# Optimization experiments

Hardware: AMD Instinct MI355X
Metric: run time of the kernel (lower is better)

## Reference

```python
import math
import jax, jax.numpy as jnp
import numpy as np

NQ = 10      # n_qubits
NB = 4       # n_blocks (angle encoding layers)
VD = 6       # vqc_depth (hardware-efficient layers)
LAT = 128    # latent_dim
NOBS = 9     # n_qubits - k_local + 1 sliding 2-local groups
DIM = 2 ** NQ


def sin_embed(t, dim):
    half = dim // 2
    freqs = jnp.exp(-math.log(10000.0) * jnp.arange(half, dtype=jnp.float32) / half)
    args = t[:, None] * freqs[None, :]
    return jnp.concatenate([jnp.cos(args), jnp.sin(args)], axis=-1)


def apply_ry(psi, theta, q):
    # psi: [B, 2^NQ] complex; theta: scalar or [B]
    B = psi.shape[0]
    p = psi.reshape(B, 2 ** q, 2, 2 ** (NQ - 1 - q))
    th = jnp.broadcast_to(theta, (B,))
    c = jnp.cos(th / 2)[:, None, None].astype(psi.dtype)
    s = jnp.sin(th / 2)[:, None, None].astype(psi.dtype)
    p0, p1 = p[:, :, 0, :], p[:, :, 1, :]
    return jnp.stack([c * p0 - s * p1, s * p0 + c * p1], axis=2).reshape(B, -1)


def apply_cnot(psi, ctrl, tgt):
    B = psi.shape[0]
    pt = psi.reshape((B,) + (2,) * NQ)
    p0 = jax.lax.index_in_dim(pt, 0, axis=ctrl + 1, keepdims=True)
    p1 = jnp.flip(jax.lax.index_in_dim(pt, 1, axis=ctrl + 1, keepdims=True), axis=tgt + 1)
    return jnp.concatenate([p0, p1], axis=ctrl + 1).reshape(B, -1)


def run_circuit(enc, var_params):
    B = enc.shape[0]
    psi = jnp.zeros((B, DIM), dtype=jnp.complex64).at[:, 0].set(1.0)
    # angle encoding: RY data re-uploading blocks with CNOT ladders between blocks
    for layer in range(NB):
        for q in range(NQ):
            psi = apply_ry(psi, enc[:, layer * NQ + q], q)
        if layer < NB - 1:
            for q in range(0, NQ - 1, 2):
                psi = apply_cnot(psi, q, q + 1)
            for q in range(1, NQ - 1, 2):
                psi = apply_cnot(psi, q, q + 1)
    # hardware-efficient variational layers
    for ly in range(VD):
        for q in range(NQ):
            psi = apply_ry(psi, var_params[ly, q], q)
        for q in range(0, NQ - 1, 2):
            psi = apply_cnot(psi, q, q + 1)
        for q in range(1, NQ - 1, 2):
            psi = apply_cnot(psi, q, q + 1)
    return psi


def build_H(A_p, B_p, D_p):
    # create_Hermitian: lower-tri (row-major) = A + iB; h[i-1,i-1] = D[i]; H = h + h^dagger
    r, c = np.tril_indices(4, -1)  # order matches count+j loop: (1,0),(2,0),(2,1),(3,0),(3,1),(3,2)
    L = jnp.zeros((NOBS, 4, 4), dtype=jnp.complex64)
    L = L.at[:, r, c].set(A_p.astype(jnp.complex64) + 1j * B_p.astype(jnp.complex64))
    d = 2.0 * jnp.concatenate([D_p[:, 1:4], jnp.zeros((NOBS, 1), dtype=D_p.dtype)], axis=1)
    H = L + jnp.conj(jnp.swapaxes(L, 1, 2))
    H = H + jax.vmap(jnp.diag)(d).astype(jnp.complex64)
    return H


def expvals(psi, H):
    B = psi.shape[0]
    outs = []
    for s in range(NOBS):  # sliding window [s, s+1]
        pg = psi.reshape(B, 2 ** s, 4, 2 ** (NQ - s - 2))
        outs.append(jnp.einsum('balr,lk,bakr->b', jnp.conj(pg), H[s], pg).real)
    return jnp.stack(outs, axis=-1)


def setup_inputs() -> dict:
    ks = jax.random.split(jax.random.key(0), 12)
    B = 2048
    return {
        'z_t': jax.random.normal(ks[0], (B, LAT), dtype=jnp.float32),
        't': jax.random.uniform(ks[1], (B,), dtype=jnp.float32),
        'W1': 0.05 * jax.random.normal(ks[2], (2 * LAT, 256), dtype=jnp.float32),
        'b1': jnp.zeros((256,), dtype=jnp.float32),
        'W2': 0.05 * jax.random.normal(ks[3], (256, NB * NQ), dtype=jnp.float32),
        'b2': jnp.zeros((NB * NQ,), dtype=jnp.float32),
        'var_params': 0.01 * jax.random.normal(ks[4], (VD, NQ), dtype=jnp.float32),
        'A_p': 2.0 * jax.random.normal(ks[5], (NOBS, 6), dtype=jnp.float32),
        'B_p': 2.0 * jax.random.normal(ks[6], (NOBS, 6), dtype=jnp.float32),
        'D_p': 2.0 * jax.random.normal(ks[7], (NOBS, 4), dtype=jnp.float32),
        'W3': 0.05 * jax.random.normal(ks[8], (NOBS, 256), dtype=jnp.float32),
        'b3': jnp.zeros((256,), dtype=jnp.float32),
        'W4': 0.05 * jax.random.normal(ks[9], (256, LAT), dtype=jnp.float32),
        'b4': jnp.zeros((LAT,), dtype=jnp.float32),
    }


def reference(z_t, t, W1, b1, W2, b2, var_params, A_p, B_p, D_p, W3, b3, W4, b4):
    x = jnp.concatenate([z_t, sin_embed(t, LAT)], axis=-1)   # [B, 2*LAT]
    h = jax.nn.silu(x @ W1 + b1)
    enc = h @ W2 + b2                                         # [B, NB*NQ]
    psi = run_circuit(enc, var_params)                        # [B, 2^NQ]
    obs = expvals(psi, build_H(A_p, B_p, D_p))                # [B, NOBS]
    return jax.nn.silu(obs @ W3 + b3) @ W4 + b4               # [B, LAT]
```

## Files before the change

### kernel.cpp

```cpp
#include <hip/hip_runtime.h>
#include <math.h>

#define NOBS 9
#define LATD 128

typedef float f2 __attribute__((ext_vector_type(2)));

__device__ __forceinline__ float silu_f(float x) { return x / (1.f + expf(-x)); }
__device__ __forceinline__ f2 splat2(float x) { return (f2){x, x}; }
__device__ __forceinline__ f2 fma2(f2 a, f2 b, f2 c) { return __builtin_elementwise_fma(a, b, c); }


template<int CTRL>
__device__ __forceinline__ float dpp_perm(float x) {
  return __int_as_float(__builtin_amdgcn_update_dpp(0, __float_as_int(x), CTRL, 0xF, 0xF, true));
}
template<int PAT>
__device__ __forceinline__ float ds_swz(float x) {
  return __int_as_float(__builtin_amdgcn_ds_swizzle(__float_as_int(x), PAT));
}
__device__ __forceinline__ float x4f(float x) { return ds_swz<0x101F>(x); }

__device__ __forceinline__ float wave_sum(float x) {
  x += dpp_perm<0xB1>(x);
  x += dpp_perm<0x4E>(x);
  x += x4f(x);
  x += dpp_perm<0x128>(x);
  x += ds_swz<0x401F>(x);
  x += __shfl_xor(x, 32, 64);
  return x;
}


template<int M>
__device__ __forceinline__ void ry_reg(float v[16], float c, float s) {
#pragma unroll
  for (int r = 0; r < 16; ++r) {
    if ((r & M) == 0) {
      float p0 = v[r], p1 = v[r | M];
      v[r]     = c * p0 - s * p1;
      v[r | M] = s * p0 + c * p1;
    }
  }
}

__device__ __forceinline__ void apply_rys(float v[16], int lane,
                                          const float* __restrict__ cc,
                                          const float* __restrict__ ss) {
  ry_reg<8>(v, cc[0], ss[0]);
  ry_reg<4>(v, cc[1], ss[1]);
  ry_reg<2>(v, cc[2], ss[2]);
  ry_reg<1>(v, cc[3], ss[3]);
  { float c = cc[4], s = ss[4], sp = (lane & 32) ? s : -s;
#pragma unroll
    for (int r = 0; r < 16; ++r) { float p = __shfl_xor(v[r], 32, 64); v[r] = fmaf(c, v[r], sp * p); } }
  { float c = cc[5], s = ss[5], sp = (lane & 16) ? s : -s;
#pragma unroll
    for (int r = 0; r < 16; ++r) { float p = __shfl_xor(v[r], 16, 64); v[r] = fmaf(c, v[r], sp * p); } }
  { float c = cc[6], s = ss[6], sp = (lane & 8) ? s : -s;
#pragma unroll
    for (int r = 0; r < 16; ++r) { float p = dpp_perm<0x128>(v[r]); v[r] = fmaf(c, v[r], sp * p); } }
  { float c = cc[7], s = ss[7], sp = (lane & 4) ? s : -s;
#pragma unroll
    for (int r = 0; r < 16; ++r) { float p = x4f(v[r]); v[r] = fmaf(c, v[r], sp * p); } }
  { float c = cc[8], s = ss[8], sp = (lane & 2) ? s : -s;
#pragma unroll
    for (int r = 0; r < 16; ++r) { float p = dpp_perm<0x4E>(v[r]); v[r] = fmaf(c, v[r], sp * p); } }
  { float c = cc[9], s = ss[9], sp = (lane & 1) ? s : -s;
#pragma unroll
    for (int r = 0; r < 16; ++r) { float p = dpp_perm<0xB1>(v[r]); v[r] = fmaf(c, v[r], sp * p); } }
}

__device__ __forceinline__ void cnot_ladder(float v[16], int lane) {
  float t;
  t=v[8];  v[8]=v[12];  v[12]=t;
  t=v[9];  v[9]=v[13];  v[13]=t;
  t=v[10]; v[10]=v[14]; v[14]=t;
  t=v[11]; v[11]=v[15]; v[15]=t;
  t=v[2];  v[2]=v[3];   v[3]=t;
  t=v[6];  v[6]=v[7];   v[7]=t;
  t=v[10]; v[10]=v[11]; v[11]=t;
  t=v[14]; v[14]=v[15]; v[15]=t;
  int se = lane ^ ((lane & 42) >> 1);
#pragma unroll
  for (int r = 0; r < 16; ++r) v[r] = __shfl(v[r], se, 64);
  t=v[4];  v[4]=v[6];   v[6]=t;
  t=v[5];  v[5]=v[7];   v[7]=t;
  t=v[12]; v[12]=v[14]; v[14]=t;
  t=v[13]; v[13]=v[15]; v[15]=t;
  int so  = lane ^ ((lane & 20) >> 1);
  int so1 = so ^ 32;
#pragma unroll
  for (int r = 0; r < 16; ++r) v[r] = __shfl(v[r], (r & 1) ? so1 : so, 64);
}


__global__ __launch_bounds__(256) void fused_kernel(
    const float* __restrict__ z, const float* __restrict__ t,
    const float* __restrict__ W1, const float* __restrict__ b1,
    const float* __restrict__ W2, const float* __restrict__ b2,
    const float* __restrict__ varp,
    const float* __restrict__ A_p, const float* __restrict__ D_p,
    const float* __restrict__ W3, const float* __restrict__ b3,
    const float* __restrict__ W4, const float* __restrict__ b4,
    float* __restrict__ out) {
  __shared__ f2    xsA[256], xsB[256];
  __shared__ float hs[4][256];
  __shared__ f2    hp[2][256];
  __shared__ float dump[4][1024];
  __shared__ float cs[4][40], sn[4][40];
  __shared__ float vcs[60], vsn[60];
  __shared__ float os[4][NOBS];

  int tid = threadIdx.x;
  int b0 = blockIdx.x * 4;

  if (tid < 60) {
    float s, c;
    sincosf(0.5f * varp[tid], &s, &c);
    vcs[tid] = c; vsn[tid] = s;
  }

  if (tid < 128) {
#pragma unroll
    for (int r = 0; r < 4; ++r) {
      float val = z[(b0 + r) * 128 + tid];
      if (r < 2) ((float*)xsA)[2 * tid + r]       = val;
      else       ((float*)xsB)[2 * tid + (r - 2)] = val;
    }
  } else {
    int i = tid - 128, j = i & 63;
    float freq = expf(-9.2103403719761836f * (float)j * (1.f / 64.f));
#pragma unroll
    for (int r = 0; r < 4; ++r) {
      float arg = t[b0 + r] * freq;
      float val = (i < 64) ? cosf(arg) : sinf(arg);
      int k = 128 + i;
      if (r < 2) ((float*)xsA)[2 * k + r]       = val;
      else       ((float*)xsB)[2 * k + (r - 2)] = val;
    }
  }
  __syncthreads();

  {
    f2 a01 = splat2(b1[tid]), a23 = a01;
    float w[16];
#pragma unroll
    for (int j = 0; j < 16; ++j) w[j] = W1[j * 256 + tid];
#pragma unroll 1
    for (int k0 = 0; k0 < 256; k0 += 16) {
      int kn = (k0 + 16) & 255;
      float wn[16];
#pragma unroll
      for (int j = 0; j < 16; ++j) wn[j] = W1[(kn + j) * 256 + tid];
#pragma unroll
      for (int j = 0; j < 16; ++j) {
        a01 = fma2(xsA[k0 + j], splat2(w[j]), a01);
        a23 = fma2(xsB[k0 + j], splat2(w[j]), a23);
      }
#pragma unroll
      for (int j = 0; j < 16; ++j) w[j] = wn[j];
    }
    hs[0][tid] = silu_f(a01.x);
    hs[1][tid] = silu_f(a01.y);
    hs[2][tid] = silu_f(a23.x);
    hs[3][tid] = silu_f(a23.y);
  }
  __syncthreads();

  if (tid < 160) {
    int r = tid / 40, c = tid - r * 40;
    float acc = b2[c];
    float w[16];
#pragma unroll
    for (int j = 0; j < 16; ++j) w[j] = W2[j * 40 + c];
#pragma unroll 1
    for (int k0 = 0; k0 < 256; k0 += 16) {
      int kn = (k0 + 16) & 255;
      float wn[16];
#pragma unroll
      for (int j = 0; j < 16; ++j) wn[j] = W2[(kn + j) * 40 + c];
#pragma unroll
      for (int j = 0; j < 16; ++j) acc = fmaf(hs[r][k0 + j], w[j], acc);
#pragma unroll
      for (int j = 0; j < 16; ++j) w[j] = wn[j];
    }
    float s, cv;
    sincosf(0.5f * acc, &s, &cv);
    cs[r][c] = cv; sn[r][c] = s;
  }
  __syncthreads();

  {
    int wave = tid >> 6;
    int lane = tid & 63;
    const float* cc = cs[wave];
    const float* ss = sn[wave];

    float base = 1.f;
    base *= (lane & 32) ? ss[4] : cc[4];
    base *= (lane & 16) ? ss[5] : cc[5];
    base *= (lane & 8)  ? ss[6] : cc[6];
    base *= (lane & 4)  ? ss[7] : cc[7];
    base *= (lane & 2)  ? ss[8] : cc[8];
    base *= (lane & 1)  ? ss[9] : cc[9];
    float v[16];
#pragma unroll
    for (int r = 0; r < 16; ++r) {
      float p = base;
      p *= (r & 8) ? ss[0] : cc[0];
      p *= (r & 4) ? ss[1] : cc[1];
      p *= (r & 2) ? ss[2] : cc[2];
      p *= (r & 1) ? ss[3] : cc[3];
      v[r] = p;
    }
    cnot_ladder(v, lane);
#pragma unroll 1
    for (int layer = 1; layer < 4; ++layer) {
      apply_rys(v, lane, cc + layer * 10, ss + layer * 10);
      if (layer < 3) cnot_ladder(v, lane);
    }
#pragma unroll 1
    for (int ly = 0; ly < 6; ++ly) {
      apply_rys(v, lane, vcs + ly * 10, vsn + ly * 10);
      cnot_ladder(v, lane);
    }

    float* sw = dump[wave];
#pragma unroll
    for (int r = 0; r < 16; ++r) sw[r * 64 + lane] = v[r];

#pragma unroll 1
    for (int s = 0; s < NOBS; ++s) {
      const int r8 = 8 - s;
      const int stride = 1 << r8;
      float h10 = A_p[s*6+0], h20 = A_p[s*6+1], h21 = A_p[s*6+2];
      float h30 = A_p[s*6+3], h31 = A_p[s*6+4], h32 = A_p[s*6+5];
      float d0 = 2.f * D_p[s*4+1], d1 = 2.f * D_p[s*4+2], d2 = 2.f * D_p[s*4+3];
      float acc = 0.f;
#pragma unroll
      for (int k = 0; k < 4; ++k) {
        int p = lane + 64 * k;
        int a  = p >> r8;
        int rr = p & (stride - 1);
        int bse = (a << (r8 + 2)) + rr;
        float x0 = sw[bse];
        float x1 = sw[bse + stride];
        float x2 = sw[bse + 2 * stride];
        float x3 = sw[bse + 3 * stride];
        acc += d0 * x0 * x0 + d1 * x1 * x1 + d2 * x2 * x2
             + 2.f * (h10 * x1 * x0 + h20 * x2 * x0 + h21 * x2 * x1
                    + h30 * x3 * x0 + h31 * x3 * x1 + h32 * x3 * x2);
      }
      acc = wave_sum(acc);
      if (lane == 0) os[wave][s] = acc;
    }
  }
  __syncthreads();

  {
    f2 a01 = splat2(b3[tid]), a23 = a01;
#pragma unroll
    for (int s = 0; s < NOBS; ++s) {
      float wv = W3[s * 256 + tid];
      a01 = fma2((f2){os[0][s], os[1][s]}, splat2(wv), a01);
      a23 = fma2((f2){os[2][s], os[3][s]}, splat2(wv), a23);
    }
    hp[0][tid] = (f2){silu_f(a01.x), silu_f(a01.y)};
    hp[1][tid] = (f2){silu_f(a23.x), silu_f(a23.y)};
  }
  __syncthreads();

  {
    int c = tid & 127, rg = tid >> 7;
    const f2* hr = hp[rg];
    f2 acc = splat2(b4[c]);
    float w[16];
#pragma unroll
    for (int j = 0; j < 16; ++j) w[j] = W4[j * 128 + c];
#pragma unroll 1
    for (int k0 = 0; k0 < 256; k0 += 16) {
      int kn = (k0 + 16) & 255;
      float wn[16];
#pragma unroll
      for (int j = 0; j < 16; ++j) wn[j] = W4[(kn + j) * 128 + c];
#pragma unroll
      for (int j = 0; j < 16; ++j) acc = fma2(hr[k0 + j], splat2(w[j]), acc);
#pragma unroll
      for (int j = 0; j < 16; ++j) w[j] = wn[j];
    }
    out[(b0 + rg * 2) * LATD + c]     = acc.x;
    out[(b0 + rg * 2 + 1) * LATD + c] = acc.y;
  }
}


extern "C" void kernel_launch(void* const* d_in, const int* in_sizes, int n_in,
                              void* d_out, int out_size, void* d_ws, size_t ws_size,
                              hipStream_t stream) {
  const float* z_t  = (const float*)d_in[0];
  const float* t    = (const float*)d_in[1];
  const float* W1   = (const float*)d_in[2];
  const float* b1   = (const float*)d_in[3];
  const float* W2   = (const float*)d_in[4];
  const float* b2   = (const float*)d_in[5];
  const float* varp = (const float*)d_in[6];
  const float* A_p  = (const float*)d_in[7];
  const float* D_p  = (const float*)d_in[9];
  const float* W3   = (const float*)d_in[10];
  const float* b3   = (const float*)d_in[11];
  const float* W4   = (const float*)d_in[12];
  const float* b4   = (const float*)d_in[13];
  float* out = (float*)d_out;

  int B = in_sizes[1];

  fused_kernel<<<B / 4, 256, 0, stream>>>(z_t, t, W1, b1, W2, b2, varp,
                                          A_p, D_p, W3, b3, W4, b4, out);
}
```

Measured before the change: 124.2 us.

## Stream weights into LDS via async global_load_lds ring buffers and split W4 over K

Weights W1, W2, W3 and W4 are now copied with global_load_lds into one flat LDS arena. W1 and W4 stream through a three-slot per-wave ring gated by vmcnt waits, instead of register double-buffering from global memory. The W4 GEMV is split across waves by K halves, with partial sums reduced through LDS, so all four waves work on it. LDS regions are aliased (the state dump reuses the W2 region) and launch bounds ask for two blocks per CU. The aim is to hide global load latency and cut register pressure, at the cost of fragile manual waitcnt scheduling and a larger LDS footprint.

After: 132.0 us. 1.06x slower.

```diff
diff --git a/kernel.cpp b/kernel.cpp
--- a/kernel.cpp
+++ b/kernel.cpp
@@ -1,8 +1,8 @@
 #include <hip/hip_runtime.h>
 #include <math.h>
+#include <stdint.h>
 
 #define NOBS 9
-#define LATD 128
 
 typedef float f2 __attribute__((ext_vector_type(2)));
 
@@ -10,6 +10,16 @@
 __device__ __forceinline__ f2 splat2(float x) { return (f2){x, x}; }
 __device__ __forceinline__ f2 fma2(f2 a, f2 b, f2 c) { return __builtin_elementwise_fma(a, b, c); }
 
+typedef const __attribute__((address_space(1))) uint32_t* gas_t;
+typedef __attribute__((address_space(3))) uint32_t* las_t;
+__device__ __forceinline__ void gl4(const float* g, float* l) {
+  __builtin_amdgcn_global_load_lds((gas_t)g, (las_t)l, 4, 0, 0);
+}
+__device__ __forceinline__ void gl16(const float* g, float* l) {
+  __builtin_amdgcn_global_load_lds((gas_t)g, (las_t)l, 16, 0, 0);
+}
+#define WAITVM(N) do { asm volatile("s_waitcnt vmcnt(" #N ")" ::: "memory"); \
+                       __builtin_amdgcn_sched_barrier(0); } while (0)
 
 template<int CTRL>
 __device__ __forceinline__ float dpp_perm(float x) {
@@ -30,7 +40,6 @@
   x += __shfl_xor(x, 32, 64);
   return x;
 }
-
 
 template<int M>
 __device__ __forceinline__ void ry_reg(float v[16], float c, float s) {
@@ -94,8 +103,22 @@
   for (int r = 0; r < 16; ++r) v[r] = __shfl(v[r], (r & 1) ? so1 : so, 64);
 }
 
-
-__global__ __launch_bounds__(256) void fused_kernel(
+#define RING 0
+#define XS   6144
+#define HS   7168
+#define W2O  8192
+#define W3O  12288
+#define HP4O 14592
+#define PARTO 15616
+#define CS   18432
+#define SN   18592
+#define VCS  18752
+#define VSN  18816
+#define OSB  18880
+#define LDSF 18944
+
+
+__global__ __launch_bounds__(256, 2) void fused_kernel(
     const float* __restrict__ z, const float* __restrict__ t,
     const float* __restrict__ W1, const float* __restrict__ b1,
     const float* __restrict__ W2, const float* __restrict__ b2,
@@ -104,98 +127,111 @@
     const float* __restrict__ W3, const float* __restrict__ b3,
     const float* __restrict__ W4, const float* __restrict__ b4,
     float* __restrict__ out) {
-  __shared__ f2    xsA[256], xsB[256];
-  __shared__ float hs[4][256];
-  __shared__ f2    hp[2][256];
-  __shared__ float dump[4][1024];
-  __shared__ float cs[4][40], sn[4][40];
-  __shared__ float vcs[60], vsn[60];
-  __shared__ float os[4][NOBS];
-
-  int tid = threadIdx.x;
-  int b0 = blockIdx.x * 4;
-
+  __shared__ __align__(16) float lds[LDSF];
+  float4* xs4 = (float4*)(lds + XS);
+  float4* hp4 = (float4*)(lds + HP4O);
+  float4* part4 = (float4*)(lds + PARTO);
+
+  const int tid  = threadIdx.x;
+  const int b0   = blockIdx.x * 4;
+  const int w    = tid >> 6;
+  const int lane = tid & 63;
+  const int c0   = w * 64;
+  const int ringw = w * 1536;
+
+  if (tid < 128) {
+    int k = tid;
+    xs4[k] = (float4){z[(b0 + 0) * 128 + k], z[(b0 + 1) * 128 + k],
+                      z[(b0 + 2) * 128 + k], z[(b0 + 3) * 128 + k]};
+  } else {
+    int i = tid - 128, j = i & 63;
+    float freq = expf(-9.2103403719761836f * (float)j * (1.f / 64.f));
+    float a0 = t[b0] * freq, a1 = t[b0 + 1] * freq, a2 = t[b0 + 2] * freq, a3 = t[b0 + 3] * freq;
+    float4 xv = (i < 64) ? (float4){cosf(a0), cosf(a1), cosf(a2), cosf(a3)}
+                         : (float4){sinf(a0), sinf(a1), sinf(a2), sinf(a3)};
+    xs4[128 + i] = xv;
+  }
   if (tid < 60) {
     float s, c;
     sincosf(0.5f * varp[tid], &s, &c);
-    vcs[tid] = c; vsn[tid] = s;
-  }
-
-  if (tid < 128) {
-#pragma unroll
-    for (int r = 0; r < 4; ++r) {
-      float val = z[(b0 + r) * 128 + tid];
-      if (r < 2) ((float*)xsA)[2 * tid + r]       = val;
-      else       ((float*)xsB)[2 * tid + (r - 2)] = val;
-    }
-  } else {
-    int i = tid - 128, j = i & 63;
-    float freq = expf(-9.2103403719761836f * (float)j * (1.f / 64.f));
-#pragma unroll
-    for (int r = 0; r < 4; ++r) {
-      float arg = t[b0 + r] * freq;
-      float val = (i < 64) ? cosf(arg) : sinf(arg);
-      int k = 128 + i;
-      if (r < 2) ((float*)xsA)[2 * k + r]       = val;
-      else       ((float*)xsB)[2 * k + (r - 2)] = val;
-    }
+    lds[VCS + tid] = c; lds[VSN + tid] = s;
   }
   __syncthreads();
 
   {
-    f2 a01 = splat2(b1[tid]), a23 = a01;
-    float w[16];
-#pragma unroll
-    for (int j = 0; j < 16; ++j) w[j] = W1[j * 256 + tid];
-#pragma unroll 1
-    for (int k0 = 0; k0 < 256; k0 += 16) {
-      int kn = (k0 + 16) & 255;
-      float wn[16];
-#pragma unroll
-      for (int j = 0; j < 16; ++j) wn[j] = W1[(kn + j) * 256 + tid];
-#pragma unroll
-      for (int j = 0; j < 16; ++j) {
-        a01 = fma2(xsA[k0 + j], splat2(w[j]), a01);
-        a23 = fma2(xsB[k0 + j], splat2(w[j]), a23);
+#pragma unroll
+    for (int q = 0; q < 10; ++q) {
+      int i = w * 10 + q;
+      gl16(W2 + i * 256 + lane * 4, lds + W2O + i * 256);
+    }
+#pragma unroll
+    for (int k = 0; k < 16; ++k)
+      gl4(W1 + k * 256 + c0 + lane, lds + ringw + k * 64);
+
+    f2 a01 = splat2(b1[c0 + lane]), a23 = a01;
+    int sbi = 2, sbp = 0;
+#pragma unroll 1
+    for (int kb = 0; kb < 30; ++kb) {
+      int kbase = (kb + 2) * 8;
+#pragma unroll
+      for (int j = 0; j < 8; ++j)
+        gl4(W1 + (kbase + j) * 256 + c0 + lane, lds + ringw + (sbi * 8 + j) * 64);
+      WAITVM(16);
+#pragma unroll
+      for (int j = 0; j < 8; ++j) {
+        float wv = lds[ringw + (sbp * 8 + j) * 64 + lane];
+        float4 x = xs4[kb * 8 + j];
+        a01 = fma2((f2){x.x, x.y}, splat2(wv), a01);
+        a23 = fma2((f2){x.z, x.w}, splat2(wv), a23);
       }
-#pragma unroll
-      for (int j = 0; j < 16; ++j) w[j] = wn[j];
-    }
-    hs[0][tid] = silu_f(a01.x);
-    hs[1][tid] = silu_f(a01.y);
-    hs[2][tid] = silu_f(a23.x);
-    hs[3][tid] = silu_f(a23.y);
+      sbi = (sbi == 2) ? 0 : sbi + 1;
+      sbp = (sbp == 2) ? 0 : sbp + 1;
+    }
+    WAITVM(8);
+#pragma unroll
+    for (int j = 0; j < 8; ++j) {
+      float wv = lds[ringw + (sbp * 8 + j) * 64 + lane];
+      float4 x = xs4[240 + j];
+      a01 = fma2((f2){x.x, x.y}, splat2(wv), a01);
+      a23 = fma2((f2){x.z, x.w}, splat2(wv), a23);
+    }
+    sbp = (sbp == 2) ? 0 : sbp + 1;
+    WAITVM(0);
+#pragma unroll
+    for (int j = 0; j < 8; ++j) {
+      float wv = lds[ringw + (sbp * 8 + j) * 64 + lane];
+      float4 x = xs4[248 + j];
+      a01 = fma2((f2){x.x, x.y}, splat2(wv), a01);
+      a23 = fma2((f2){x.z, x.w}, splat2(wv), a23);
+    }
+    int c = c0 + lane;
+    lds[HS + 0 * 256 + c] = silu_f(a01.x);
+    lds[HS + 1 * 256 + c] = silu_f(a01.y);
+    lds[HS + 2 * 256 + c] = silu_f(a23.x);
+    lds[HS + 3 * 256 + c] = silu_f(a23.y);
   }
   __syncthreads();
 
   if (tid < 160) {
     int r = tid / 40, c = tid - r * 40;
     float acc = b2[c];
-    float w[16];
-#pragma unroll
-    for (int j = 0; j < 16; ++j) w[j] = W2[j * 40 + c];
-#pragma unroll 1
-    for (int k0 = 0; k0 < 256; k0 += 16) {
-      int kn = (k0 + 16) & 255;
-      float wn[16];
-#pragma unroll
-      for (int j = 0; j < 16; ++j) wn[j] = W2[(kn + j) * 40 + c];
-#pragma unroll
-      for (int j = 0; j < 16; ++j) acc = fmaf(hs[r][k0 + j], w[j], acc);
-#pragma unroll
-      for (int j = 0; j < 16; ++j) w[j] = wn[j];
-    }
+#pragma unroll 8
+    for (int k = 0; k < 256; ++k)
+      acc = fmaf(lds[HS + r * 256 + k], lds[W2O + k * 40 + c], acc);
     float s, cv;
     sincosf(0.5f * acc, &s, &cv);
-    cs[r][c] = cv; sn[r][c] = s;
-  }
-  __syncthreads();
-
+    lds[CS + r * 40 + c] = cv;
+    lds[SN + r * 40 + c] = s;
+  }
+  __syncthreads();
+
+  for (int i = w; i < 9; i += 4)
+    gl16(W3 + i * 256 + lane * 4, lds + W3O + i * 256);
   {
-    int wave = tid >> 6;
-    int lane = tid & 63;
-    const float* cc = cs[wave];
-    const float* ss = sn[wave];
+    const float* cc = lds + CS + w * 40;
+    const float* ss = lds + SN + w * 40;
+    const float* vcs = lds + VCS;
+    const float* vsn = lds + VSN;
 
     float base = 1.f;
     base *= (lane & 32) ? ss[4] : cc[4];
@@ -226,7 +262,7 @@
       cnot_ladder(v, lane);
     }
 
-    float* sw = dump[wave];
+    float* sw = lds + W2O + w * 1024;
 #pragma unroll
     for (int r = 0; r < 16; ++r) sw[r * 64 + lane] = v[r];
 
@@ -253,44 +289,78 @@
                     + h30 * x3 * x0 + h31 * x3 * x1 + h32 * x3 * x2);
       }
       acc = wave_sum(acc);
-      if (lane == 0) os[wave][s] = acc;
+      if (lane == 0) lds[OSB + w * 9 + s] = acc;
     }
   }
   __syncthreads();
 
   {
-    f2 a01 = splat2(b3[tid]), a23 = a01;
+    int col = tid;
+    f2 q01 = splat2(b3[col]), q23 = q01;
 #pragma unroll
     for (int s = 0; s < NOBS; ++s) {
-      float wv = W3[s * 256 + tid];
-      a01 = fma2((f2){os[0][s], os[1][s]}, splat2(wv), a01);
-      a23 = fma2((f2){os[2][s], os[3][s]}, splat2(wv), a23);
-    }
-    hp[0][tid] = (f2){silu_f(a01.x), silu_f(a01.y)};
-    hp[1][tid] = (f2){silu_f(a23.x), silu_f(a23.y)};
+      float wv = lds[W3O + s * 256 + col];
+      q01 = fma2((f2){lds[OSB + 0 * 9 + s], lds[OSB + 1 * 9 + s]}, splat2(wv), q01);
+      q23 = fma2((f2){lds[OSB + 2 * 9 + s], lds[OSB + 3 * 9 + s]}, splat2(wv), q23);
+    }
+    hp4[col] = (float4){silu_f(q01.x), silu_f(q01.y), silu_f(q23.x), silu_f(q23.y)};
   }
   __syncthreads();
 
   {
-    int c = tid & 127, rg = tid >> 7;
-    const f2* hr = hp[rg];
-    f2 acc = splat2(b4[c]);
-    float w[16];
-#pragma unroll
-    for (int j = 0; j < 16; ++j) w[j] = W4[j * 128 + c];
-#pragma unroll 1
-    for (int k0 = 0; k0 < 256; k0 += 16) {
-      int kn = (k0 + 16) & 255;
-      float wn[16];
-#pragma unroll
-      for (int j = 0; j < 16; ++j) wn[j] = W4[(kn + j) * 128 + c];
-#pragma unroll
-      for (int j = 0; j < 16; ++j) acc = fma2(hr[k0 + j], splat2(w[j]), acc);
-#pragma unroll
-      for (int j = 0; j < 16; ++j) w[j] = wn[j];
-    }
-    out[(b0 + rg * 2) * LATD + c]     = acc.x;
-    out[(b0 + rg * 2 + 1) * LATD + c] = acc.y;
+    const int c0b = (w & 1) * 64;
+    const int kh  = (w >> 1) * 128;
+#pragma unroll
+    for (int kl = 0; kl < 16; ++kl)
+      gl4(W4 + (kh + kl) * 128 + c0b + lane, lds + ringw + kl * 64);
+
+    f2 a01 = splat2(0.f), a23 = splat2(0.f);
+    int sbi = 2, sbp = 0;
+#pragma unroll 1
+    for (int kb = 0; kb < 14; ++kb) {
+      int kbase = (kb + 2) * 8;
+#pragma unroll
+      for (int j = 0; j < 8; ++j)
+        gl4(W4 + (kh + kbase + j) * 128 + c0b + lane, lds + ringw + (sbi * 8 + j) * 64);
+      WAITVM(16);
+#pragma unroll
+      for (int j = 0; j < 8; ++j) {
+        float wv = lds[ringw + (sbp * 8 + j) * 64 + lane];
+        float4 h = hp4[kh + kb * 8 + j];
+        a01 = fma2((f2){h.x, h.y}, splat2(wv), a01);
+        a23 = fma2((f2){h.z, h.w}, splat2(wv), a23);
+      }
+      sbi = (sbi == 2) ? 0 : sbi + 1;
+      sbp = (sbp == 2) ? 0 : sbp + 1;
+    }
+    WAITVM(8);
+#pragma unroll
+    for (int j = 0; j < 8; ++j) {
+      float wv = lds[ringw + (sbp * 8 + j) * 64 + lane];
+      float4 h = hp4[kh + 112 + j];
+      a01 = fma2((f2){h.x, h.y}, splat2(wv), a01);
+      a23 = fma2((f2){h.z, h.w}, splat2(wv), a23);
+    }
+    sbp = (sbp == 2) ? 0 : sbp + 1;
+    WAITVM(0);
+#pragma unroll
+    for (int j = 0; j < 8; ++j) {
+      float wv = lds[ringw + (sbp * 8 + j) * 64 + lane];
+      float4 h = hp4[kh + 120 + j];
+      a01 = fma2((f2){h.x, h.y}, splat2(wv), a01);
+      a23 = fma2((f2){h.z, h.w}, splat2(wv), a23);
+    }
+    if (w >= 2) part4[(w - 2) * 64 + lane] = (float4){a01.x, a01.y, a23.x, a23.y};
+    __syncthreads();
+    if (w < 2) {
+      float4 p = part4[w * 64 + lane];
+      int c = c0b + lane;
+      float bb = b4[c];
+      out[(b0 + 0) * 128 + c] = a01.x + p.x + bb;
+      out[(b0 + 1) * 128 + c] = a01.y + p.y + bb;
+      out[(b0 + 2) * 128 + c] = a23.x + p.z + bb;
+      out[(b0 + 3) * 128 + c] = a23.y + p.w + bb;
+    }
   }
 }
 
```

## Split fused kernel into encoder, per-sample circuit, and head kernels

Applied to the files above, without the earlier changes.

Replaces the single fused kernel with four launches: a tiny kernel for the sincos of the variational angles, an encoder MLP kernel, a circuit kernel with one 64-thread wave per sample, and a head MLP kernel. Intermediates pass through workspace memory. The aim is to shrink LDS use and barriers per block in the circuit stage so more waves fit per CU. The GEMV loops also drop manual register double-buffering in favour of plain unroll-8 loops, and inputs are packed as float4 in LDS. In exchange it adds launch overhead and global round-trips for the intermediates.

New measurement: 140.7 us. +13.3%, slower.

```diff
diff --git a/kernel.cpp b/kernel.cpp
--- a/kernel.cpp
+++ b/kernel.cpp
@@ -2,14 +2,12 @@
 #include <math.h>
 
 #define NOBS 9
-#define LATD 128
 
 typedef float f2 __attribute__((ext_vector_type(2)));
 
 __device__ __forceinline__ float silu_f(float x) { return x / (1.f + expf(-x)); }
 __device__ __forceinline__ f2 splat2(float x) { return (f2){x, x}; }
 __device__ __forceinline__ f2 fma2(f2 a, f2 b, f2 c) { return __builtin_elementwise_fma(a, b, c); }
-
 
 template<int CTRL>
 __device__ __forceinline__ float dpp_perm(float x) {
@@ -30,7 +28,6 @@
   x += __shfl_xor(x, 32, 64);
   return x;
 }
-
 
 template<int M>
 __device__ __forceinline__ void ry_reg(float v[16], float c, float s) {
@@ -94,72 +91,48 @@
   for (int r = 0; r < 16; ++r) v[r] = __shfl(v[r], (r & 1) ? so1 : so, 64);
 }
 
-
-__global__ __launch_bounds__(256) void fused_kernel(
+__global__ __launch_bounds__(64) void varcs_kernel(const float* __restrict__ varp,
+                                                   float* __restrict__ varc,
+                                                   float* __restrict__ vars) {
+  int tid = threadIdx.x;
+  if (tid < 60) {
+    float s, c;
+    sincosf(0.5f * varp[tid], &s, &c);
+    varc[tid] = c;
+    vars[tid] = s;
+  }
+}
+
+__global__ __launch_bounds__(256) void enc_kernel(
     const float* __restrict__ z, const float* __restrict__ t,
     const float* __restrict__ W1, const float* __restrict__ b1,
     const float* __restrict__ W2, const float* __restrict__ b2,
-    const float* __restrict__ varp,
-    const float* __restrict__ A_p, const float* __restrict__ D_p,
-    const float* __restrict__ W3, const float* __restrict__ b3,
-    const float* __restrict__ W4, const float* __restrict__ b4,
-    float* __restrict__ out) {
-  __shared__ f2    xsA[256], xsB[256];
+    float* __restrict__ csg, float* __restrict__ sng) {
+  __shared__ __align__(16) float4 xs4[256];
   __shared__ float hs[4][256];
-  __shared__ f2    hp[2][256];
-  __shared__ float dump[4][1024];
-  __shared__ float cs[4][40], sn[4][40];
-  __shared__ float vcs[60], vsn[60];
-  __shared__ float os[4][NOBS];
-
   int tid = threadIdx.x;
   int b0 = blockIdx.x * 4;
 
-  if (tid < 60) {
-    float s, c;
-    sincosf(0.5f * varp[tid], &s, &c);
-    vcs[tid] = c; vsn[tid] = s;
-  }
-
   if (tid < 128) {
-#pragma unroll
-    for (int r = 0; r < 4; ++r) {
-      float val = z[(b0 + r) * 128 + tid];
-      if (r < 2) ((float*)xsA)[2 * tid + r]       = val;
-      else       ((float*)xsB)[2 * tid + (r - 2)] = val;
-    }
+    xs4[tid] = (float4){z[(b0 + 0) * 128 + tid], z[(b0 + 1) * 128 + tid],
+                        z[(b0 + 2) * 128 + tid], z[(b0 + 3) * 128 + tid]};
   } else {
     int i = tid - 128, j = i & 63;
     float freq = expf(-9.2103403719761836f * (float)j * (1.f / 64.f));
-#pragma unroll
-    for (int r = 0; r < 4; ++r) {
-      float arg = t[b0 + r] * freq;
-      float val = (i < 64) ? cosf(arg) : sinf(arg);
-      int k = 128 + i;
-      if (r < 2) ((float*)xsA)[2 * k + r]       = val;
-      else       ((float*)xsB)[2 * k + (r - 2)] = val;
-    }
+    float a0 = t[b0] * freq, a1 = t[b0 + 1] * freq, a2 = t[b0 + 2] * freq, a3 = t[b0 + 3] * freq;
+    xs4[tid] = (i < 64) ? (float4){cosf(a0), cosf(a1), cosf(a2), cosf(a3)}
+                        : (float4){sinf(a0), sinf(a1), sinf(a2), sinf(a3)};
   }
   __syncthreads();
 
   {
     f2 a01 = splat2(b1[tid]), a23 = a01;
-    float w[16];
-#pragma unroll
-    for (int j = 0; j < 16; ++j) w[j] = W1[j * 256 + tid];
-#pragma unroll 1
-    for (int k0 = 0; k0 < 256; k0 += 16) {
-      int kn = (k0 + 16) & 255;
-      float wn[16];
-#pragma unroll
-      for (int j = 0; j < 16; ++j) wn[j] = W1[(kn + j) * 256 + tid];
-#pragma unroll
-      for (int j = 0; j < 16; ++j) {
-        a01 = fma2(xsA[k0 + j], splat2(w[j]), a01);
-        a23 = fma2(xsB[k0 + j], splat2(w[j]), a23);
-      }
-#pragma unroll
-      for (int j = 0; j < 16; ++j) w[j] = wn[j];
+#pragma unroll 8
+    for (int k = 0; k < 256; ++k) {
+      float wv = W1[k * 256 + tid];
+      float4 x = xs4[k];
+      a01 = fma2((f2){x.x, x.y}, splat2(wv), a01);
+      a23 = fma2((f2){x.z, x.w}, splat2(wv), a23);
     }
     hs[0][tid] = silu_f(a01.x);
     hs[1][tid] = silu_f(a01.y);
@@ -171,126 +144,122 @@
   if (tid < 160) {
     int r = tid / 40, c = tid - r * 40;
     float acc = b2[c];
-    float w[16];
-#pragma unroll
-    for (int j = 0; j < 16; ++j) w[j] = W2[j * 40 + c];
-#pragma unroll 1
-    for (int k0 = 0; k0 < 256; k0 += 16) {
-      int kn = (k0 + 16) & 255;
-      float wn[16];
-#pragma unroll
-      for (int j = 0; j < 16; ++j) wn[j] = W2[(kn + j) * 40 + c];
-#pragma unroll
-      for (int j = 0; j < 16; ++j) acc = fmaf(hs[r][k0 + j], w[j], acc);
-#pragma unroll
-      for (int j = 0; j < 16; ++j) w[j] = wn[j];
-    }
+#pragma unroll 8
+    for (int k = 0; k < 256; ++k)
+      acc = fmaf(hs[r][k], W2[k * 40 + c], acc);
     float s, cv;
     sincosf(0.5f * acc, &s, &cv);
-    cs[r][c] = cv; sn[r][c] = s;
-  }
+    csg[(b0 + r) * 40 + c] = cv;
+    sng[(b0 + r) * 40 + c] = s;
+  }
+}
+
+__global__ __launch_bounds__(64) void circuit_kernel(
+    const float* __restrict__ csg, const float* __restrict__ sng,
+    const float* __restrict__ varc, const float* __restrict__ vars,
+    const float* __restrict__ A_p, const float* __restrict__ D_p,
+    float* __restrict__ obs) {
+  __shared__ float sw[1024];
+  int lane = threadIdx.x;
+  int b = blockIdx.x;
+  const float* cc = csg + b * 40;
+  const float* ss = sng + b * 40;
+
+  float base = 1.f;
+  base *= (lane & 32) ? ss[4] : cc[4];
+  base *= (lane & 16) ? ss[5] : cc[5];
+  base *= (lane & 8)  ? ss[6] : cc[6];
+  base *= (lane & 4)  ? ss[7] : cc[7];
+  base *= (lane & 2)  ? ss[8] : cc[8];
+  base *= (lane & 1)  ? ss[9] : cc[9];
+  float v[16];
+#pragma unroll
+  for (int r = 0; r < 16; ++r) {
+    float p = base;
+    p *= (r & 8) ? ss[0] : cc[0];
+    p *= (r & 4) ? ss[1] : cc[1];
+    p *= (r & 2) ? ss[2] : cc[2];
+    p *= (r & 1) ? ss[3] : cc[3];
+    v[r] = p;
+  }
+  cnot_ladder(v, lane);
+#pragma unroll 1
+  for (int layer = 1; layer < 4; ++layer) {
+    apply_rys(v, lane, cc + layer * 10, ss + layer * 10);
+    if (layer < 3) cnot_ladder(v, lane);
+  }
+#pragma unroll 1
+  for (int ly = 0; ly < 6; ++ly) {
+    apply_rys(v, lane, varc + ly * 10, vars + ly * 10);
+    cnot_ladder(v, lane);
+  }
+
+#pragma unroll
+  for (int r = 0; r < 16; ++r) sw[r * 64 + lane] = v[r];
+
+#pragma unroll 1
+  for (int s = 0; s < NOBS; ++s) {
+    const int r8 = 8 - s;
+    const int stride = 1 << r8;
+    float h10 = A_p[s*6+0], h20 = A_p[s*6+1], h21 = A_p[s*6+2];
+    float h30 = A_p[s*6+3], h31 = A_p[s*6+4], h32 = A_p[s*6+5];
+    float d0 = 2.f * D_p[s*4+1], d1 = 2.f * D_p[s*4+2], d2 = 2.f * D_p[s*4+3];
+    float acc = 0.f;
+#pragma unroll
+    for (int k = 0; k < 4; ++k) {
+      int p = lane + 64 * k;
+      int a  = p >> r8;
+      int rr = p & (stride - 1);
+      int bse = (a << (r8 + 2)) + rr;
+      float x0 = sw[bse];
+      float x1 = sw[bse + stride];
+      float x2 = sw[bse + 2 * stride];
+      float x3 = sw[bse + 3 * stride];
+      acc += d0 * x0 * x0 + d1 * x1 * x1 + d2 * x2 * x2
+           + 2.f * (h10 * x1 * x0 + h20 * x2 * x0 + h21 * x2 * x1
+                  + h30 * x3 * x0 + h31 * x3 * x1 + h32 * x3 * x2);
+    }
+    acc = wave_sum(acc);
+    if (lane == 0) obs[b * NOBS + s] = acc;
+  }
+}
+
+__global__ __launch_bounds__(256) void head_kernel(
+    const float* __restrict__ obs, const float* __restrict__ W3,
+    const float* __restrict__ b3, const float* __restrict__ W4,
+    const float* __restrict__ b4, float* __restrict__ out) {
+  __shared__ float os[4][NOBS];
+  __shared__ __align__(16) float4 hp4[256];
+  int tid = threadIdx.x;
+  int b0 = blockIdx.x * 4;
+
+  if (tid < 4 * NOBS) os[tid / NOBS][tid % NOBS] = obs[b0 * NOBS + tid];
   __syncthreads();
 
   {
-    int wave = tid >> 6;
-    int lane = tid & 63;
-    const float* cc = cs[wave];
-    const float* ss = sn[wave];
-
-    float base = 1.f;
-    base *= (lane & 32) ? ss[4] : cc[4];
-    base *= (lane & 16) ? ss[5] : cc[5];
-    base *= (lane & 8)  ? ss[6] : cc[6];
-    base *= (lane & 4)  ? ss[7] : cc[7];
-    base *= (lane & 2)  ? ss[8] : cc[8];
-    base *= (lane & 1)  ? ss[9] : cc[9];
-    float v[16];
-#pragma unroll
-    for (int r = 0; r < 16; ++r) {
-      float p = base;
-      p *= (r & 8) ? ss[0] : cc[0];
-      p *= (r & 4) ? ss[1] : cc[1];
-      p *= (r & 2) ? ss[2] : cc[2];
-      p *= (r & 1) ? ss[3] : cc[3];
-      v[r] = p;
-    }
-    cnot_ladder(v, lane);
-#pragma unroll 1
-    for (int layer = 1; layer < 4; ++layer) {
-      apply_rys(v, lane, cc + layer * 10, ss + layer * 10);
-      if (layer < 3) cnot_ladder(v, lane);
-    }
-#pragma unroll 1
-    for (int ly = 0; ly < 6; ++ly) {
-      apply_rys(v, lane, vcs + ly * 10, vsn + ly * 10);
-      cnot_ladder(v, lane);
-    }
-
-    float* sw = dump[wave];
-#pragma unroll
-    for (int r = 0; r < 16; ++r) sw[r * 64 + lane] = v[r];
-
-#pragma unroll 1
-    for (int s = 0; s < NOBS; ++s) {
-      const int r8 = 8 - s;
-      const int stride = 1 << r8;
-      float h10 = A_p[s*6+0], h20 = A_p[s*6+1], h21 = A_p[s*6+2];
-      float h30 = A_p[s*6+3], h31 = A_p[s*6+4], h32 = A_p[s*6+5];
-      float d0 = 2.f * D_p[s*4+1], d1 = 2.f * D_p[s*4+2], d2 = 2.f * D_p[s*4+3];
-      float acc = 0.f;
-#pragma unroll
-      for (int k = 0; k < 4; ++k) {
-        int p = lane + 64 * k;
-        int a  = p >> r8;
-        int rr = p & (stride - 1);
-        int bse = (a << (r8 + 2)) + rr;
-        float x0 = sw[bse];
-        float x1 = sw[bse + stride];
-        float x2 = sw[bse + 2 * stride];
-        float x3 = sw[bse + 3 * stride];
-        acc += d0 * x0 * x0 + d1 * x1 * x1 + d2 * x2 * x2
-             + 2.f * (h10 * x1 * x0 + h20 * x2 * x0 + h21 * x2 * x1
-                    + h30 * x3 * x0 + h31 * x3 * x1 + h32 * x3 * x2);
-      }
-      acc = wave_sum(acc);
-      if (lane == 0) os[wave][s] = acc;
-    }
-  }
-  __syncthreads();
-
-  {
-    f2 a01 = splat2(b3[tid]), a23 = a01;
+    f2 q01 = splat2(b3[tid]), q23 = q01;
 #pragma unroll
     for (int s = 0; s < NOBS; ++s) {
       float wv = W3[s * 256 + tid];
-      a01 = fma2((f2){os[0][s], os[1][s]}, splat2(wv), a01);
-      a23 = fma2((f2){os[2][s], os[3][s]}, splat2(wv), a23);
-    }
-    hp[0][tid] = (f2){silu_f(a01.x), silu_f(a01.y)};
-    hp[1][tid] = (f2){silu_f(a23.x), silu_f(a23.y)};
+      q01 = fma2((f2){os[0][s], os[1][s]}, splat2(wv), q01);
+      q23 = fma2((f2){os[2][s], os[3][s]}, splat2(wv), q23);
+    }
+    hp4[tid] = (float4){silu_f(q01.x), silu_f(q01.y), silu_f(q23.x), silu_f(q23.y)};
   }
   __syncthreads();
 
   {
     int c = tid & 127, rg = tid >> 7;
-    const f2* hr = hp[rg];
     f2 acc = splat2(b4[c]);
-    float w[16];
-#pragma unroll
-    for (int j = 0; j < 16; ++j) w[j] = W4[j * 128 + c];
-#pragma unroll 1
-    for (int k0 = 0; k0 < 256; k0 += 16) {
-      int kn = (k0 + 16) & 255;
-      float wn[16];
-#pragma unroll
-      for (int j = 0; j < 16; ++j) wn[j] = W4[(kn + j) * 128 + c];
-#pragma unroll
-      for (int j = 0; j < 16; ++j) acc = fma2(hr[k0 + j], splat2(w[j]), acc);
-#pragma unroll
-      for (int j = 0; j < 16; ++j) w[j] = wn[j];
-    }
-    out[(b0 + rg * 2) * LATD + c]     = acc.x;
-    out[(b0 + rg * 2 + 1) * LATD + c] = acc.y;
+#pragma unroll 8
+    for (int k = 0; k < 256; ++k) {
+      float wv = W4[k * 128 + c];
+      float4 h = hp4[k];
+      f2 hp = (rg == 0) ? (f2){h.x, h.y} : (f2){h.z, h.w};
+      acc = fma2(hp, splat2(wv), acc);
+    }
+    out[(b0 + 2 * rg) * 128 + c]     = acc.x;
+    out[(b0 + 2 * rg + 1) * 128 + c] = acc.y;
   }
 }
 
@@ -315,6 +284,14 @@
 
   int B = in_sizes[1];
 
-  fused_kernel<<<B / 4, 256, 0, stream>>>(z_t, t, W1, b1, W2, b2, varp,
-                                          A_p, D_p, W3, b3, W4, b4, out);
-}
+  float* csg  = (float*)d_ws;
+  float* sng  = csg + (size_t)B * 40;
+  float* obs  = sng + (size_t)B * 40;
+  float* varc = obs + (size_t)B * 9;
+  float* vars = varc + 64;
+
+  varcs_kernel<<<1, 64, 0, stream>>>(varp, varc, vars);
+  enc_kernel<<<B / 4, 256, 0, stream>>>(z_t, t, W1, b1, W2, b2, csg, sng);
+  circuit_kernel<<<B, 64, 0, stream>>>(csg, sng, varc, vars, A_p, D_p, obs);
+  head_kernel<<<B / 4, 256, 0, stream>>>(obs, W3, b3, W4, b4, out);
+}
```
